# Kernel optimization log

Measured on AMD Instinct MI355X. Metric: run time of the kernel, lower is better.

The kernel has to match this reference:

```python
import jax, jax.numpy as jnp
import numpy as np

EPSILON = 0.01            # params.epsilon (cluster precision regularizer)
GAMMA = 0.005             # params.gamma (outlier/uniform component weight)
FIX_CLUSTER_POS_ITER = 1  # params.fix_cluster_pos_iter


def _sqdist(TVs, X):
    # TVs: (M, 3, N) transformed points, X: (K, 3) cluster means -> (M, N, K)
    return ((TVs ** 2).sum(1)[:, :, None]
            + (X ** 2).sum(1)[None, None, :]
            - 2.0 * jnp.einsum('mdn,kd->mnk', TVs, X))


def setup_inputs() -> dict:
    key = jax.random.key(0)
    kV, kX, kQ = jax.random.split(key, 3)
    M, N, K = 8, 8192, 256
    Vs = jax.random.normal(kV, (M, 3, N), dtype=jnp.float32)      # 3D point clouds
    X0 = jax.random.normal(kX, (K, 3), dtype=jnp.float32)         # init cluster means (sphere init)
    Q0 = 0.1 + 0.2 * jax.random.uniform(kQ, (K,), dtype=jnp.float32)  # init cluster precisions
    return {"Vs": Vs, "X0": X0, "Q0": Q0, "num_iters": 6}


def reference(Vs, X0, Q0, num_iters):
    M, _, N = Vs.shape
    K = X0.shape[0]
    dtype = Vs.dtype

    # mean_init: init_R = I, init_t = -mean(V) per view
    t0 = -Vs.mean(axis=2, keepdims=True)          # (M, 3, 1)
    TVs = Vs + t0
    beta = GAMMA * jnp.mean(Q0) ** 1.5            # get_default_beta(Q, gamma)

    X, Q = X0, Q0
    ds = _sqdist(TVs, X)                          # (M, N, K)
    R = jnp.broadcast_to(jnp.eye(3, dtype=dtype), (M, 3, 3))
    t = t0[:, :, 0]

    for i in range(num_iters):
        if i != num_iters - 1:  # detach everything except backprop_iter = [last]
            X = jax.lax.stop_gradient(X)
            Q = jax.lax.stop_gradient(Q)
            ds = jax.lax.stop_gradient(ds)

        # E-step: soft posteriors with uniform outlier component beta
        ap = jnp.exp(-0.5 * ds * Q) * Q ** 1.5    # (M, N, K); priors = 1, pyz_feature = 1
        a = ap / (ap.sum(axis=-1, keepdims=True) + beta)

        # M-step: weighted sufficient statistics
        L = a.sum(axis=1)                                   # (M, K)
        W = jnp.einsum('mdn,mnk->mdk', Vs, a) * Q           # (M, 3, K)
        mW = W.sum(axis=-1)                                 # (M, 3)
        b = L * Q                                           # (M, K)
        mX = jnp.einsum('mk,kd->md', b, X)                  # (M, 3)
        z = b.sum(axis=-1)                                  # (M,)

        # P = (W @ X)^T - mX mW^T / z  : 3x3 weighted cross-covariance per view
        P = (jnp.einsum('mdk,ke->med', W, X)
             - mX[:, :, None] * mW[:, None, :] / z[:, None, None])

        # batched Procrustes: R = U diag(1,1,det(U V^T)) V^T
        U, _, Vt = jnp.linalg.svd(P)
        det = jnp.linalg.det(jnp.einsum('mij,mjk->mik', U, Vt))
        sgn = jnp.concatenate([jnp.ones((M, 2), dtype), det[:, None]], axis=1)
        R = jnp.einsum('mij,mjk->mik', U * sgn[:, None, :], Vt)   # (M, 3, 3)
        t = (mX - jnp.einsum('mij,mj->mi', R, mW)) / z[:, None]   # (M, 3)
        TVs = jnp.einsum('mij,mjn->min', R, Vs) + t[:, :, None]   # (M, 3, N)

        # shared cluster updates (sum over views)
        den = L.sum(axis=0)                                 # (K,)
        if i > FIX_CLUSTER_POS_ITER:
            X = jnp.einsum('mdn,mnk->kd', TVs, a) / den[:, None]
        ds = _sqdist(TVs, X)
        wn = (a * ds).sum(axis=(0, 1))                      # (K,)
        Q = 3.0 * den / (wn + 3.0 * den * EPSILON)

    return TVs, R, t, X
```

## Files before the change

kernel.cpp:

```cpp
#include <hip/hip_runtime.h>
#include <math.h>

#define Mv 8
#define Nv 8192
#define Kv 256
#define BPM 64
#define NBLK (Mv*BPM)
#define NITER 6
#define EPSILON_C 0.01f
#define GAMMA_C 0.005f

#define WS_R     0
#define WS_T     72
#define WS_X     96
#define WS_Q     864
#define WS_BETA  1120
#define WS_ACC   1124
#define AC_STATS 0
#define AC_L     128
#define AC_W     2176
#define AC_H     8320
#define ACCSZ    10368

__device__ __forceinline__ float wave_red_sum(float x) {
  int v;
  float t;
  v = __builtin_bit_cast(int, x);
  t = __builtin_bit_cast(float, __builtin_amdgcn_update_dpp(0, v, 0x111, 0xf, 0xf, true));
  x += t; v = __builtin_bit_cast(int, x);
  t = __builtin_bit_cast(float, __builtin_amdgcn_update_dpp(0, v, 0x112, 0xf, 0xf, true));
  x += t; v = __builtin_bit_cast(int, x);
  t = __builtin_bit_cast(float, __builtin_amdgcn_update_dpp(0, v, 0x114, 0xf, 0xf, true));
  x += t; v = __builtin_bit_cast(int, x);
  t = __builtin_bit_cast(float, __builtin_amdgcn_update_dpp(0, v, 0x118, 0xf, 0xf, true));
  x += t; v = __builtin_bit_cast(int, x);
  t = __builtin_bit_cast(float, __builtin_amdgcn_update_dpp(0, v, 0x142, 0xa, 0xf, false));
  x += t; v = __builtin_bit_cast(int, x);
  t = __builtin_bit_cast(float, __builtin_amdgcn_update_dpp(0, v, 0x143, 0xc, 0xf, false));
  x += t;
  return __builtin_bit_cast(float, __builtin_amdgcn_readlane(__builtin_bit_cast(int, x), 63));
}

__global__ __launch_bounds__(256) void p0_init(const float* __restrict__ Vs,
                                               const float* __restrict__ X0,
                                               const float* __restrict__ Q0,
                                               float* __restrict__ ws) {
  __shared__ float sred[4];
  int tid = threadIdx.x;
  int b = blockIdx.x;
  int wave = tid >> 6, lane = tid & 63;
  if (b < 24) {
    int m = b / 3, d = b % 3;
    const float* src = Vs + (size_t)(m*3 + d) * Nv;
    float s = 0.f;
    for (int n = tid; n < Nv; n += 256) s += src[n];
    s = wave_red_sum(s);
    if (lane == 0) sred[wave] = s;
    __syncthreads();
    if (tid == 0) {
      float tot = sred[0]+sred[1]+sred[2]+sred[3];
      ws[WS_T + m*3 + d] = -tot / (float)Nv;
    }
    if (d == 0 && tid < 9) {
      ws[WS_R + m*9 + tid] = (tid==0||tid==4||tid==8) ? 1.f : 0.f;
    }
  } else {
    float s = (tid < Kv) ? Q0[tid] : 0.f;
    s = wave_red_sum(s);
    if (lane == 0) sred[wave] = s;
    __syncthreads();
    if (tid == 0) {
      float mq = (sred[0]+sred[1]+sred[2]+sred[3]) / (float)Kv;
      ws[WS_BETA] = GAMMA_C * mq * sqrtf(mq);
    }
    if (tid < Kv) ws[WS_Q + tid] = Q0[tid];
    for (int i = tid; i < Kv*3; i += 256) ws[WS_X + i] = X0[i];
    for (int i = tid; i < ACCSZ; i += 256) ws[WS_ACC + i] = 0.f;
  }
}

#define JROTF(app,aqq,apq,apr,aqr, vp0,vp1,vp2, vq0,vq1,vq2) do {           \
    float tau_ = (aqq - app) * __builtin_amdgcn_rcpf(2.0f*apq);             \
    float tt_ = __builtin_amdgcn_rcpf(fabsf(tau_) +                         \
                   __builtin_amdgcn_sqrtf(fmaf(tau_,tau_,1.0f)));           \
    tt_ = (tau_ < 0.0f) ? -tt_ : tt_;                                       \
    tt_ = (apq == 0.0f) ? 0.0f : tt_;                                       \
    float c_ = __builtin_amdgcn_rsqf(fmaf(tt_,tt_,1.0f)), s_ = tt_*c_;      \
    float papq_ = apq;                                                      \
    app = fmaf(-tt_,papq_,app); aqq = fmaf(tt_,papq_,aqq); apq = 0.0f;      \
    float tp_ = apr, tq_ = aqr;                                             \
    apr = c_*tp_ - s_*tq_; aqr = s_*tp_ + c_*tq_;                           \
    tp_=vp0; tq_=vq0; vp0=c_*tp_-s_*tq_; vq0=s_*tp_+c_*tq_;                 \
    tp_=vp1; tq_=vq1; vp1=c_*tp_-s_*tq_; vq1=s_*tp_+c_*tq_;                 \
    tp_=vp2; tq_=vq2; vp2=c_*tp_-s_*tq_; vq2=s_*tp_+c_*tq_;                 \
  } while(0)

#define CSWAP3F(la,lb, a0,a1,a2, b0,b1,b2) do {                             \
    if (la < lb) { float t_;                                                \
      t_=la; la=lb; lb=t_; t_=a0; a0=b0; b0=t_;                             \
      t_=a1; a1=b1; b1=t_; t_=a2; a2=b2; b2=t_; }                           \
  } while(0)

template<int ITPREV>
__device__ __forceinline__ void small_update(const float* __restrict__ acc,
                                             const float* __restrict__ ws,
                                             int tid,
                                             float (*sX)[3], float* sQ,
                                             float (*sR)[9], float (*sT)[3],
                                             float* sTn) {
  const int k = tid;
  float lk[Mv], w0v[Mv], w1v[Mv], w2v[Mv], hk[Mv];
  #pragma unroll
  for (int mm=0;mm<Mv;mm++) {
    lk[mm]  = acc[AC_L + mm*Kv + k];
    w0v[mm] = acc[AC_W + (mm*3+0)*Kv + k];
    w1v[mm] = acc[AC_W + (mm*3+1)*Kv + k];
    w2v[mm] = acc[AC_W + (mm*3+2)*Kv + k];
    hk[mm]  = acc[AC_H + mm*Kv + k];
  }
  float xp0 = 0.f, xp1 = 0.f, xp2 = 0.f;
  if (ITPREV <= 1) {
    xp0 = ws[WS_X + k*3+0]; xp1 = ws[WS_X + k*3+1]; xp2 = ws[WS_X + k*3+2];
  }

  if (tid < Mv) {
    int mm = tid;
    const float* st = acc + AC_STATS + mm*16;
    float s0=st[0], s1=st[1], s2v=st[2], s3=st[3], s4=st[4], s5=st[5],
          s6=st[6], s7=st[7], s8=st[8], s9=st[9], s10=st[10], s11=st[11],
          s12=st[12], s13=st[13], s14=st[14], s15=st[15];
    float z = s0;
    float mX0 = s1, mX1 = s2v, mX2 = s3;
    float mW0 = s4, mW1 = s5, mW2 = s6;
    float iz = __builtin_amdgcn_rcpf(z);
    float P00 = s7  - mX0*mW0*iz;
    float P01 = s8  - mX0*mW1*iz;
    float P02 = s9  - mX0*mW2*iz;
    float P10 = s10 - mX1*mW0*iz;
    float P11 = s11 - mX1*mW1*iz;
    float P12 = s12 - mX1*mW2*iz;
    float P20 = s13 - mX2*mW0*iz;
    float P21 = s14 - mX2*mW1*iz;
    float P22 = s15 - mX2*mW2*iz;
    float a00 = P00*P00 + P10*P10 + P20*P20;
    float a01 = P00*P01 + P10*P11 + P20*P21;
    float a02 = P00*P02 + P10*P12 + P20*P22;
    float a11 = P01*P01 + P11*P11 + P21*P21;
    float a12 = P01*P02 + P11*P12 + P21*P22;
    float a22 = P02*P02 + P12*P12 + P22*P22;
    float v00=1, v01=0, v02=0, v10=0, v11=1, v12=0, v20=0, v21=0, v22=1;
    #pragma unroll 1
    for (int sweep = 0; sweep < 8; sweep++) {
      JROTF(a00,a11,a01, a02,a12, v00,v10,v20, v01,v11,v21);
      JROTF(a00,a22,a02, a01,a12, v00,v10,v20, v02,v12,v22);
      JROTF(a11,a22,a12, a01,a02, v01,v11,v21, v02,v12,v22);
    }
    float l0 = a00, l1 = a11, l2 = a22;
    CSWAP3F(l0,l1, v00,v10,v20, v01,v11,v21);
    CSWAP3F(l1,l2, v01,v11,v21, v02,v12,v22);
    CSWAP3F(l0,l1, v00,v10,v20, v01,v11,v21);
    float detP = P00*(P11*P22-P12*P21) - P01*(P10*P22-P12*P20)
               + P02*(P10*P21-P11*P20);
    float s2d = (detP < 0.0f) ? -1.0f : 1.0f;
    float tiny = 1e-18f*l0 + 1e-30f;
    float w0i = __builtin_amdgcn_rsqf(fmaxf(l0,tiny));
    float w1i = __builtin_amdgcn_rsqf(fmaxf(l1,tiny));
    float w2i = s2d*__builtin_amdgcn_rsqf(fmaxf(l2,tiny));
    float M00 = w0i*v00*v00 + w1i*v01*v01 + w2i*v02*v02;
    float M01 = w0i*v00*v10 + w1i*v01*v11 + w2i*v02*v12;
    float M02 = w0i*v00*v20 + w1i*v01*v21 + w2i*v02*v22;
    float M11 = w0i*v10*v10 + w1i*v11*v11 + w2i*v12*v12;
    float M12 = w0i*v10*v20 + w1i*v11*v21 + w2i*v12*v22;
    float M22 = w0i*v20*v20 + w1i*v21*v21 + w2i*v22*v22;
    float R00n = P00*M00 + P01*M01 + P02*M02;
    float R01n = P00*M01 + P01*M11 + P02*M12;
    float R02n = P00*M02 + P01*M12 + P02*M22;
    float R10n = P10*M00 + P11*M01 + P12*M02;
    float R11n = P10*M01 + P11*M11 + P12*M12;
    float R12n = P10*M02 + P11*M12 + P12*M22;
    float R20n = P20*M00 + P21*M01 + P22*M02;
    float R21n = P20*M01 + P21*M11 + P22*M12;
    float R22n = P20*M02 + P21*M12 + P22*M22;
    float tm0 = (mX0 - (R00n*mW0 + R01n*mW1 + R02n*mW2))*iz;
    float tm1 = (mX1 - (R10n*mW0 + R11n*mW1 + R12n*mW2))*iz;
    float tm2 = (mX2 - (R20n*mW0 + R21n*mW1 + R22n*mW2))*iz;
    sR[mm][0]=R00n; sR[mm][1]=R01n; sR[mm][2]=R02n;
    sR[mm][3]=R10n; sR[mm][4]=R11n; sR[mm][5]=R12n;
    sR[mm][6]=R20n; sR[mm][7]=R21n; sR[mm][8]=R22n;
    sT[mm][0]=tm0; sT[mm][1]=tm1; sT[mm][2]=tm2;
    sTn[mm] = tm0*tm0 + tm1*tm1 + tm2*tm2;
  }
  __syncthreads();
  {
    float den = 0.f, Xn0=0.f, Xn1=0.f, Xn2=0.f, S2=0.f;
    #pragma unroll
    for (int mm=0;mm<Mv;mm++) {
      float r0 = sR[mm][0]*w0v[mm] + sR[mm][1]*w1v[mm] + sR[mm][2]*w2v[mm];
      float r1 = sR[mm][3]*w0v[mm] + sR[mm][4]*w1v[mm] + sR[mm][5]*w2v[mm];
      float r2 = sR[mm][6]*w0v[mm] + sR[mm][7]*w1v[mm] + sR[mm][8]*w2v[mm];
      float tt0 = sT[mm][0], tt1 = sT[mm][1], tt2 = sT[mm][2];
      den += lk[mm];
      Xn0 += r0 + tt0*lk[mm]; Xn1 += r1 + tt1*lk[mm]; Xn2 += r2 + tt2*lk[mm];
      S2  += hk[mm] + 2.f*(tt0*r0+tt1*r1+tt2*r2) + sTn[mm]*lk[mm];
    }
    float x0, x1, x2;
    if (ITPREV > 1) { float inv = __builtin_amdgcn_rcpf(den);
                      x0=Xn0*inv; x1=Xn1*inv; x2=Xn2*inv; }
    else            { x0=xp0; x1=xp1; x2=xp2; }
    float wn = S2 + (x0*x0+x1*x1+x2*x2)*den - 2.f*(x0*Xn0+x1*Xn1+x2*Xn2);
    float qn = 3.f*den / (wn + 3.f*den*EPSILON_C);
    sX[k][0]=x0; sX[k][1]=x1; sX[k][2]=x2;
    sQ[k] = qn;
  }
}

template<int IT>
__global__ __launch_bounds__(256) void p_iter(const float* __restrict__ Vs,
                                              float* __restrict__ ws) {
  __shared__ float sb[4][5][Kv];
  __shared__ float st4[4][16];
  __shared__ float sX[Kv][3];
  __shared__ float sQ[Kv];
  __shared__ float sR[Mv][9];
  __shared__ float sT[Mv][3];
  __shared__ float sTn[Mv];

  int tid  = threadIdx.x;
  int wave = tid >> 6, lane = tid & 63;
  int bid  = blockIdx.x;
  int m    = bid / BPM;
  int blk  = bid % BPM;
  int wid  = blk*4 + wave;
  const int k = tid;

  float* acc  = ws + WS_ACC + (IT % 3)*ACCSZ;
  float* accz = ws + WS_ACC + ((IT+1) % 3)*ACCSZ;
  float beta = ws[WS_BETA];

  if (IT == 0) {
    if (tid < 72) ((float*)sR)[tid] = ws[WS_R + tid];
    if (tid < 24) ((float*)sT)[tid] = ws[WS_T + tid];
    sX[k][0] = ws[WS_X + 3*k+0];
    sX[k][1] = ws[WS_X + 3*k+1];
    sX[k][2] = ws[WS_X + 3*k+2];
    sQ[k]    = ws[WS_Q + k];
  } else {
    const float* accp = ws + WS_ACC + ((IT+2) % 3)*ACCSZ;
    small_update<(IT > 0) ? (IT-1) : 0>(accp, ws, tid, sX, sQ, sR, sT, sTn);
  }
  __syncthreads();

  { int base = bid*21;
    if (tid < 21 && base + tid < ACCSZ) accz[base + tid] = 0.f; }

  float R00=sR[m][0],R01=sR[m][1],R02=sR[m][2];
  float R10=sR[m][3],R11=sR[m][4],R12=sR[m][5];
  float R20=sR[m][6],R21=sR[m][7],R22=sR[m][8];
  float t0=sT[m][0], t1=sT[m][1], t2=sT[m][2];
  float kXx[4],kXy[4],kXz[4],kA[4],kB[4],kQ[4],kQ32[4];
  #pragma unroll
  for (int j=0;j<4;j++) {
    int kk = lane + 64*j;
    float xx = sX[kk][0], xy = sX[kk][1], xz = sX[kk][2];
    float q  = sQ[kk];
    kXx[j]=xx; kXy[j]=xy; kXz[j]=xz;
    kA[j]  = -0.5f*q;
    kB[j]  = kA[j]*(xx*xx+xy*xy+xz*xz);
    kQ[j]  = q;
    kQ32[j]= q*sqrtf(q);
  }
  float aL[4]={0,0,0,0}, aWx[4]={0,0,0,0}, aWy[4]={0,0,0,0},
        aWz[4]={0,0,0,0}, aH[4]={0,0,0,0};
  const float* V0 = Vs + (size_t)(m*3+0)*Nv;
  const float* V1 = Vs + (size_t)(m*3+1)*Nv;
  const float* V2 = Vs + (size_t)(m*3+2)*Nv;
  for (int n = wid; n < Nv; n += 256) {
    float vx = V0[n], vy = V1[n], vz = V2[n];
    float px = fmaf(R00,vx, fmaf(R01,vy, fmaf(R02,vz, t0)));
    float py = fmaf(R10,vx, fmaf(R11,vy, fmaf(R12,vz, t1)));
    float pz = fmaf(R20,vx, fmaf(R21,vy, fmaf(R22,vz, t2)));
    float tvn = fmaf(px,px, fmaf(py,py, pz*pz));
    float vn  = fmaf(vx,vx, fmaf(vy,vy, vz*vz));
    float ap[4]; float s = 0.f;
    #pragma unroll
    for (int j=0;j<4;j++) {
      float dot = fmaf(px,kXx[j], fmaf(py,kXy[j], pz*kXz[j]));
      float arg = fmaf(kQ[j], dot, fmaf(kA[j], tvn, kB[j]));
      float e = __expf(arg)*kQ32[j];
      ap[j] = e; s += e;
    }
    float S = wave_red_sum(s);
    float inv = __builtin_amdgcn_rcpf(S + beta);
    #pragma unroll
    for (int j=0;j<4;j++) {
      float a = ap[j]*inv;
      aL[j] += a;
      aWx[j] = fmaf(a,vx,aWx[j]);
      aWy[j] = fmaf(a,vy,aWy[j]);
      aWz[j] = fmaf(a,vz,aWz[j]);
      aH[j]  = fmaf(a,vn,aH[j]);
    }
  }
  #pragma unroll
  for (int j=0;j<4;j++) {
    int kk = lane + 64*j;
    sb[wave][0][kk]=aL[j];  sb[wave][1][kk]=aWx[j]; sb[wave][2][kk]=aWy[j];
    sb[wave][3][kk]=aWz[j]; sb[wave][4][kk]=aH[j];
  }
  __syncthreads();
  const int k2 = (tid + 4*blk) & (Kv-1);
  float vL  = sb[0][0][k2]+sb[1][0][k2]+sb[2][0][k2]+sb[3][0][k2];
  float vWx = sb[0][1][k2]+sb[1][1][k2]+sb[2][1][k2]+sb[3][1][k2];
  float vWy = sb[0][2][k2]+sb[1][2][k2]+sb[2][2][k2]+sb[3][2][k2];
  float vWz = sb[0][3][k2]+sb[1][3][k2]+sb[2][3][k2]+sb[3][3][k2];
  float vH  = sb[0][4][k2]+sb[1][4][k2]+sb[2][4][k2]+sb[3][4][k2];
  atomicAdd(&acc[AC_L + m*Kv + k2], vL);
  atomicAdd(&acc[AC_W + (m*3+0)*Kv + k2], vWx);
  atomicAdd(&acc[AC_W + (m*3+1)*Kv + k2], vWy);
  atomicAdd(&acc[AC_W + (m*3+2)*Kv + k2], vWz);
  atomicAdd(&acc[AC_H + m*Kv + k2], vH);
  {
    float q  = sQ[k2];
    float x0 = sX[k2][0], x1 = sX[k2][1], x2 = sX[k2][2];
    float bk = vL*q;
    float sw0 = vWx*q, sw1 = vWy*q, sw2 = vWz*q;
    float pr[16];
    pr[0]=bk;  pr[1]=bk*x0; pr[2]=bk*x1; pr[3]=bk*x2;
    pr[4]=sw0; pr[5]=sw1;   pr[6]=sw2;
    pr[7]=sw0*x0;  pr[8]=sw1*x0;  pr[9]=sw2*x0;
    pr[10]=sw0*x1; pr[11]=sw1*x1; pr[12]=sw2*x1;
    pr[13]=sw0*x2; pr[14]=sw1*x2; pr[15]=sw2*x2;
    float red[16];
    #pragma unroll
    for (int v2=0; v2<16; v2++) red[v2] = wave_red_sum(pr[v2]);
    if (lane == 0) {
      #pragma unroll
      for (int v2=0; v2<16; v2++) st4[wave][v2] = red[v2];
    }
    __syncthreads();
    if (tid < 16)
      atomicAdd(&acc[AC_STATS + m*16 + ((tid + blk) & 15)],
                st4[0][(tid+blk)&15]+st4[1][(tid+blk)&15]+
                st4[2][(tid+blk)&15]+st4[3][(tid+blk)&15]);
  }
}

#define OUT_TOTAL (Mv*3*Nv + 72 + 24 + Kv*3)
__global__ __launch_bounds__(256) void p3_final(const float* __restrict__ Vs,
                                                const float* __restrict__ ws,
                                                float* __restrict__ out) {
  __shared__ float sX[Kv][3];
  __shared__ float sQ[Kv];
  __shared__ float sR[Mv][9];
  __shared__ float sT[Mv][3];
  __shared__ float sTn[Mv];
  int tid = threadIdx.x;
  const float* acc = ws + WS_ACC + ((NITER-1) % 3)*ACCSZ;
  small_update<NITER-1>(acc, ws, tid, sX, sQ, sR, sT, sTn);
  __syncthreads();

  for (int idx = blockIdx.x*256 + tid; idx < OUT_TOTAL; idx += 256*256) {
    if (idx < Mv*3*Nv) {
      int m = idx / (3*Nv);
      int r = idx % (3*Nv);
      int d = r / Nv;
      int n = r % Nv;
      float vx = Vs[(size_t)(m*3+0)*Nv + n];
      float vy = Vs[(size_t)(m*3+1)*Nv + n];
      float vz = Vs[(size_t)(m*3+2)*Nv + n];
      out[idx] = fmaf(sR[m][d*3+0],vx,
                 fmaf(sR[m][d*3+1],vy,
                 fmaf(sR[m][d*3+2],vz, sT[m][d])));
    } else {
      int j = idx - Mv*3*Nv;
      float v;
      if (j < 72)      v = ((float*)sR)[j];
      else if (j < 96) v = ((float*)sT)[j-72];
      else             v = ((float*)sX)[j-96];
      out[idx] = v;
    }
  }
}

extern "C" void kernel_launch(void* const* d_in, const int* in_sizes, int n_in,
                              void* d_out, int out_size, void* d_ws, size_t ws_size,
                              hipStream_t stream) {
  const float* Vs = (const float*)d_in[0];
  const float* X0 = (const float*)d_in[1];
  const float* Q0 = (const float*)d_in[2];
  float* out = (float*)d_out;
  float* ws  = (float*)d_ws;

  p0_init<<<25, 256, 0, stream>>>(Vs, X0, Q0, ws);
  p_iter<0><<<NBLK, 256, 0, stream>>>(Vs, ws);
  p_iter<1><<<NBLK, 256, 0, stream>>>(Vs, ws);
  p_iter<2><<<NBLK, 256, 0, stream>>>(Vs, ws);
  p_iter<3><<<NBLK, 256, 0, stream>>>(Vs, ws);
  p_iter<4><<<NBLK, 256, 0, stream>>>(Vs, ws);
  p_iter<5><<<NBLK, 256, 0, stream>>>(Vs, ws);
  p3_final<<<256, 256, 0, stream>>>(Vs, ws, out);
}
```

Baseline: 214.0 us.

## Double blocks per view, process two points per iteration, fold log2e into constants

Raises blocks per view from 64 to 128 and adds an occupancy hint to the launch bounds. The point loop now handles two points per iteration so their wave reductions and exp calls can interleave. The exp is rewritten as a native exp2 with log2(e) and Q folded into the per-cluster constants, which drops a multiply per cluster. More blocks means more atomic traffic into the accumulators and a smaller per-block zeroing slice; the two-point loop assumes N divides evenly by the stride.

```diff
diff --git a/kernel.cpp b/kernel.cpp
--- a/kernel.cpp
+++ b/kernel.cpp
@@ -4,8 +4,9 @@
 #define Mv 8
 #define Nv 8192
 #define Kv 256
-#define BPM 64
+#define BPM 128
 #define NBLK (Mv*BPM)
+#define WSTRIDE (4*BPM)
 #define NITER 6
 #define EPSILON_C 0.01f
 #define GAMMA_C 0.005f
@@ -215,8 +216,8 @@
 }
 
 template<int IT>
-__global__ __launch_bounds__(256) void p_iter(const float* __restrict__ Vs,
-                                              float* __restrict__ ws) {
+__global__ __launch_bounds__(256, 4) void p_iter(const float* __restrict__ Vs,
+                                                 float* __restrict__ ws) {
   __shared__ float sb[4][5][Kv];
   __shared__ float st4[4][16];
   __shared__ float sX[Kv][3];
@@ -230,7 +231,7 @@
   int bid  = blockIdx.x;
   int m    = bid / BPM;
   int blk  = bid % BPM;
-  int wid  = blk*4 + wave;
+  int wid  = __builtin_amdgcn_readfirstlane(blk*4 + wave);
   const int k = tid;
 
   float* acc  = ws + WS_ACC + (IT % 3)*ACCSZ;
@@ -250,23 +251,24 @@
   }
   __syncthreads();
 
-  { int base = bid*21;
-    if (tid < 21 && base + tid < ACCSZ) accz[base + tid] = 0.f; }
+  { int base = bid*11;
+    if (tid < 11 && base + tid < ACCSZ) accz[base + tid] = 0.f; }
 
   float R00=sR[m][0],R01=sR[m][1],R02=sR[m][2];
   float R10=sR[m][3],R11=sR[m][4],R12=sR[m][5];
   float R20=sR[m][6],R21=sR[m][7],R22=sR[m][8];
   float t0=sT[m][0], t1=sT[m][1], t2=sT[m][2];
-  float kXx[4],kXy[4],kXz[4],kA[4],kB[4],kQ[4],kQ32[4];
+  const float L2E = 1.4426950408889634f;
+  float kXx[4],kXy[4],kXz[4],kA[4],kB[4],kQ32[4];
   #pragma unroll
   for (int j=0;j<4;j++) {
     int kk = lane + 64*j;
     float xx = sX[kk][0], xy = sX[kk][1], xz = sX[kk][2];
     float q  = sQ[kk];
-    kXx[j]=xx; kXy[j]=xy; kXz[j]=xz;
-    kA[j]  = -0.5f*q;
+    float qL = q * L2E;
+    kA[j]  = -0.5f*qL;
+    kXx[j] = qL*xx; kXy[j] = qL*xy; kXz[j] = qL*xz;
     kB[j]  = kA[j]*(xx*xx+xy*xy+xz*xz);
-    kQ[j]  = q;
     kQ32[j]= q*sqrtf(q);
   }
   float aL[4]={0,0,0,0}, aWx[4]={0,0,0,0}, aWy[4]={0,0,0,0},
@@ -274,31 +276,48 @@
   const float* V0 = Vs + (size_t)(m*3+0)*Nv;
   const float* V1 = Vs + (size_t)(m*3+1)*Nv;
   const float* V2 = Vs + (size_t)(m*3+2)*Nv;
-  for (int n = wid; n < Nv; n += 256) {
-    float vx = V0[n], vy = V1[n], vz = V2[n];
-    float px = fmaf(R00,vx, fmaf(R01,vy, fmaf(R02,vz, t0)));
-    float py = fmaf(R10,vx, fmaf(R11,vy, fmaf(R12,vz, t1)));
-    float pz = fmaf(R20,vx, fmaf(R21,vy, fmaf(R22,vz, t2)));
-    float tvn = fmaf(px,px, fmaf(py,py, pz*pz));
-    float vn  = fmaf(vx,vx, fmaf(vy,vy, vz*vz));
-    float ap[4]; float s = 0.f;
+  #pragma unroll 1
+  for (int i = 0; i < Nv/(2*WSTRIDE); i++) {
+    int n0 = wid + (2*WSTRIDE)*i;
+    int n1 = n0 + WSTRIDE;
+    float vx0 = V0[n0], vy0 = V1[n0], vz0 = V2[n0];
+    float vx1 = V0[n1], vy1 = V1[n1], vz1 = V2[n1];
+    float px0 = fmaf(R00,vx0, fmaf(R01,vy0, fmaf(R02,vz0, t0)));
+    float py0 = fmaf(R10,vx0, fmaf(R11,vy0, fmaf(R12,vz0, t1)));
+    float pz0 = fmaf(R20,vx0, fmaf(R21,vy0, fmaf(R22,vz0, t2)));
+    float px1 = fmaf(R00,vx1, fmaf(R01,vy1, fmaf(R02,vz1, t0)));
+    float py1 = fmaf(R10,vx1, fmaf(R11,vy1, fmaf(R12,vz1, t1)));
+    float pz1 = fmaf(R20,vx1, fmaf(R21,vy1, fmaf(R22,vz1, t2)));
+    float tvn0 = fmaf(px0,px0, fmaf(py0,py0, pz0*pz0));
+    float tvn1 = fmaf(px1,px1, fmaf(py1,py1, pz1*pz1));
+    float vn0  = fmaf(vx0,vx0, fmaf(vy0,vy0, vz0*vz0));
+    float vn1  = fmaf(vx1,vx1, fmaf(vy1,vy1, vz1*vz1));
+    float ap0[4], ap1[4];
+    float s0 = 0.f, s1 = 0.f;
     #pragma unroll
     for (int j=0;j<4;j++) {
-      float dot = fmaf(px,kXx[j], fmaf(py,kXy[j], pz*kXz[j]));
-      float arg = fmaf(kQ[j], dot, fmaf(kA[j], tvn, kB[j]));
-      float e = __expf(arg)*kQ32[j];
-      ap[j] = e; s += e;
-    }
-    float S = wave_red_sum(s);
-    float inv = __builtin_amdgcn_rcpf(S + beta);
+      float b0 = fmaf(kA[j], tvn0, kB[j]);
+      float b1 = fmaf(kA[j], tvn1, kB[j]);
+      float arg0 = fmaf(px0,kXx[j], fmaf(py0,kXy[j], fmaf(pz0,kXz[j], b0)));
+      float arg1 = fmaf(px1,kXx[j], fmaf(py1,kXy[j], fmaf(pz1,kXz[j], b1)));
+      float e0 = __builtin_amdgcn_exp2f(arg0) * kQ32[j];
+      float e1 = __builtin_amdgcn_exp2f(arg1) * kQ32[j];
+      ap0[j] = e0; s0 += e0;
+      ap1[j] = e1; s1 += e1;
+    }
+    float S0 = wave_red_sum(s0);
+    float S1 = wave_red_sum(s1);
+    float inv0 = __builtin_amdgcn_rcpf(S0 + beta);
+    float inv1 = __builtin_amdgcn_rcpf(S1 + beta);
     #pragma unroll
     for (int j=0;j<4;j++) {
-      float a = ap[j]*inv;
-      aL[j] += a;
-      aWx[j] = fmaf(a,vx,aWx[j]);
-      aWy[j] = fmaf(a,vy,aWy[j]);
-      aWz[j] = fmaf(a,vz,aWz[j]);
-      aH[j]  = fmaf(a,vn,aH[j]);
+      float a0 = ap0[j]*inv0;
+      float a1 = ap1[j]*inv1;
+      aL[j] += a0 + a1;
+      aWx[j] = fmaf(a1,vx1, fmaf(a0,vx0, aWx[j]));
+      aWy[j] = fmaf(a1,vy1, fmaf(a0,vy0, aWy[j]));
+      aWz[j] = fmaf(a1,vz1, fmaf(a0,vz0, aWz[j]));
+      aH[j]  = fmaf(a1,vn1, fmaf(a0,vn0, aH[j]));
     }
   }
   #pragma unroll
```

After: 226.3 us. 1.06x slower.

## Restructure E-step to per-point normalizer pass then per-cluster accumulation

Applied to the files above, without the earlier changes.

Replaces the wave-per-point layout, where each lane held four clusters and a cross-lane reduction ran per point, with two phases per block. In the first phase each thread owns one point and loops over all clusters read from shared memory to compute its normalizer. In the second phase each thread owns one cluster and loops over the block's points to accumulate its statistics. This removes the per-point wave reductions and the shared-memory cross-wave combine, and switches to exp2 with folded constants. In exchange the exponential is computed twice per point-cluster pair, and the block count is halved to 32 blocks per view with 256 points each.

```diff
diff --git a/kernel.cpp b/kernel.cpp
--- a/kernel.cpp
+++ b/kernel.cpp
@@ -4,8 +4,9 @@
 #define Mv 8
 #define Nv 8192
 #define Kv 256
-#define BPM 64
+#define BPM 32
 #define NBLK (Mv*BPM)
+#define NPB (Nv/BPM)
 #define NITER 6
 #define EPSILON_C 0.01f
 #define GAMMA_C 0.005f
@@ -217,7 +218,10 @@
 template<int IT>
 __global__ __launch_bounds__(256) void p_iter(const float* __restrict__ Vs,
                                               float* __restrict__ ws) {
-  __shared__ float sb[4][5][Kv];
+  __shared__ __align__(16) float sC[Kv][8];
+  __shared__ __align__(16) float sPT[NPB][4];
+  __shared__ __align__(16) float sVV[NPB][4];
+  __shared__ float sInv[NPB];
   __shared__ float st4[4][16];
   __shared__ float sX[Kv][3];
   __shared__ float sQ[Kv];
@@ -230,8 +234,7 @@
   int bid  = blockIdx.x;
   int m    = bid / BPM;
   int blk  = bid % BPM;
-  int wid  = blk*4 + wave;
-  const int k = tid;
+  int n0   = blk * NPB;
 
   float* acc  = ws + WS_ACC + (IT % 3)*ACCSZ;
   float* accz = ws + WS_ACC + ((IT+1) % 3)*ACCSZ;
@@ -240,96 +243,101 @@
   if (IT == 0) {
     if (tid < 72) ((float*)sR)[tid] = ws[WS_R + tid];
     if (tid < 24) ((float*)sT)[tid] = ws[WS_T + tid];
-    sX[k][0] = ws[WS_X + 3*k+0];
-    sX[k][1] = ws[WS_X + 3*k+1];
-    sX[k][2] = ws[WS_X + 3*k+2];
-    sQ[k]    = ws[WS_Q + k];
+    sX[tid][0] = ws[WS_X + 3*tid+0];
+    sX[tid][1] = ws[WS_X + 3*tid+1];
+    sX[tid][2] = ws[WS_X + 3*tid+2];
+    sQ[tid]    = ws[WS_Q + tid];
   } else {
     const float* accp = ws + WS_ACC + ((IT+2) % 3)*ACCSZ;
     small_update<(IT > 0) ? (IT-1) : 0>(accp, ws, tid, sX, sQ, sR, sT, sTn);
   }
   __syncthreads();
 
-  { int base = bid*21;
-    if (tid < 21 && base + tid < ACCSZ) accz[base + tid] = 0.f; }
+  { int base = bid*41;
+    if (tid < 41 && base + tid < ACCSZ) accz[base + tid] = 0.f; }
+
+  const float L2E = 1.4426950408889634f;
+  float xx = sX[tid][0], xy = sX[tid][1], xz = sX[tid][2];
+  float q  = sQ[tid];
+  float qL   = q * L2E;
+  float kA   = -0.5f*qL;
+  float kXx  = qL*xx, kXy = qL*xy, kXz = qL*xz;
+  float kB   = kA*(xx*xx+xy*xy+xz*xz);
+  float kQ32 = q*sqrtf(q);
+  sC[tid][0]=kXx; sC[tid][1]=kXy; sC[tid][2]=kXz;
+  sC[tid][3]=kA;  sC[tid][4]=kB;  sC[tid][5]=kQ32;
 
   float R00=sR[m][0],R01=sR[m][1],R02=sR[m][2];
   float R10=sR[m][3],R11=sR[m][4],R12=sR[m][5];
   float R20=sR[m][6],R21=sR[m][7],R22=sR[m][8];
   float t0=sT[m][0], t1=sT[m][1], t2=sT[m][2];
-  float kXx[4],kXy[4],kXz[4],kA[4],kB[4],kQ[4],kQ32[4];
-  #pragma unroll
-  for (int j=0;j<4;j++) {
-    int kk = lane + 64*j;
-    float xx = sX[kk][0], xy = sX[kk][1], xz = sX[kk][2];
-    float q  = sQ[kk];
-    kXx[j]=xx; kXy[j]=xy; kXz[j]=xz;
-    kA[j]  = -0.5f*q;
-    kB[j]  = kA[j]*(xx*xx+xy*xy+xz*xz);
-    kQ[j]  = q;
-    kQ32[j]= q*sqrtf(q);
-  }
-  float aL[4]={0,0,0,0}, aWx[4]={0,0,0,0}, aWy[4]={0,0,0,0},
-        aWz[4]={0,0,0,0}, aH[4]={0,0,0,0};
-  const float* V0 = Vs + (size_t)(m*3+0)*Nv;
-  const float* V1 = Vs + (size_t)(m*3+1)*Nv;
-  const float* V2 = Vs + (size_t)(m*3+2)*Nv;
-  for (int n = wid; n < Nv; n += 256) {
-    float vx = V0[n], vy = V1[n], vz = V2[n];
-    float px = fmaf(R00,vx, fmaf(R01,vy, fmaf(R02,vz, t0)));
-    float py = fmaf(R10,vx, fmaf(R11,vy, fmaf(R12,vz, t1)));
-    float pz = fmaf(R20,vx, fmaf(R21,vy, fmaf(R22,vz, t2)));
-    float tvn = fmaf(px,px, fmaf(py,py, pz*pz));
-    float vn  = fmaf(vx,vx, fmaf(vy,vy, vz*vz));
-    float ap[4]; float s = 0.f;
-    #pragma unroll
-    for (int j=0;j<4;j++) {
-      float dot = fmaf(px,kXx[j], fmaf(py,kXy[j], pz*kXz[j]));
-      float arg = fmaf(kQ[j], dot, fmaf(kA[j], tvn, kB[j]));
-      float e = __expf(arg)*kQ32[j];
-      ap[j] = e; s += e;
-    }
-    float S = wave_red_sum(s);
-    float inv = __builtin_amdgcn_rcpf(S + beta);
-    #pragma unroll
-    for (int j=0;j<4;j++) {
-      float a = ap[j]*inv;
-      aL[j] += a;
-      aWx[j] = fmaf(a,vx,aWx[j]);
-      aWy[j] = fmaf(a,vy,aWy[j]);
-      aWz[j] = fmaf(a,vz,aWz[j]);
-      aH[j]  = fmaf(a,vn,aH[j]);
-    }
-  }
-  #pragma unroll
-  for (int j=0;j<4;j++) {
-    int kk = lane + 64*j;
-    sb[wave][0][kk]=aL[j];  sb[wave][1][kk]=aWx[j]; sb[wave][2][kk]=aWy[j];
-    sb[wave][3][kk]=aWz[j]; sb[wave][4][kk]=aH[j];
-  }
+  int n = n0 + tid;
+  float vx = Vs[(size_t)(m*3+0)*Nv + n];
+  float vy = Vs[(size_t)(m*3+1)*Nv + n];
+  float vz = Vs[(size_t)(m*3+2)*Nv + n];
+  float px = fmaf(R00,vx, fmaf(R01,vy, fmaf(R02,vz, t0)));
+  float py = fmaf(R10,vx, fmaf(R11,vy, fmaf(R12,vz, t1)));
+  float pz = fmaf(R20,vx, fmaf(R21,vy, fmaf(R22,vz, t2)));
+  float tvn = fmaf(px,px, fmaf(py,py, pz*pz));
+  float vn  = fmaf(vx,vx, fmaf(vy,vy, vz*vz));
+  sPT[tid][0]=px; sPT[tid][1]=py; sPT[tid][2]=pz; sPT[tid][3]=tvn;
+  sVV[tid][0]=vx; sVV[tid][1]=vy; sVV[tid][2]=vz; sVV[tid][3]=vn;
   __syncthreads();
-  const int k2 = (tid + 4*blk) & (Kv-1);
-  float vL  = sb[0][0][k2]+sb[1][0][k2]+sb[2][0][k2]+sb[3][0][k2];
-  float vWx = sb[0][1][k2]+sb[1][1][k2]+sb[2][1][k2]+sb[3][1][k2];
-  float vWy = sb[0][2][k2]+sb[1][2][k2]+sb[2][2][k2]+sb[3][2][k2];
-  float vWz = sb[0][3][k2]+sb[1][3][k2]+sb[2][3][k2]+sb[3][3][k2];
-  float vH  = sb[0][4][k2]+sb[1][4][k2]+sb[2][4][k2]+sb[3][4][k2];
-  atomicAdd(&acc[AC_L + m*Kv + k2], vL);
-  atomicAdd(&acc[AC_W + (m*3+0)*Kv + k2], vWx);
-  atomicAdd(&acc[AC_W + (m*3+1)*Kv + k2], vWy);
-  atomicAdd(&acc[AC_W + (m*3+2)*Kv + k2], vWz);
-  atomicAdd(&acc[AC_H + m*Kv + k2], vH);
+
   {
-    float q  = sQ[k2];
-    float x0 = sX[k2][0], x1 = sX[k2][1], x2 = sX[k2][2];
-    float bk = vL*q;
-    float sw0 = vWx*q, sw1 = vWy*q, sw2 = vWz*q;
+    float s0=0.f, s1=0.f, s2=0.f, s3=0.f;
+    #pragma unroll 2
+    for (int k = 0; k < Kv; k += 4) {
+      float4 c0 = *reinterpret_cast<const float4*>(&sC[k+0][0]);
+      float2 d0 = *reinterpret_cast<const float2*>(&sC[k+0][4]);
+      float4 c1 = *reinterpret_cast<const float4*>(&sC[k+1][0]);
+      float2 d1 = *reinterpret_cast<const float2*>(&sC[k+1][4]);
+      float4 c2 = *reinterpret_cast<const float4*>(&sC[k+2][0]);
+      float2 d2 = *reinterpret_cast<const float2*>(&sC[k+2][4]);
+      float4 c3 = *reinterpret_cast<const float4*>(&sC[k+3][0]);
+      float2 d3 = *reinterpret_cast<const float2*>(&sC[k+3][4]);
+      float a0 = fmaf(px,c0.x, fmaf(py,c0.y, fmaf(pz,c0.z, fmaf(c0.w,tvn,d0.x))));
+      float a1 = fmaf(px,c1.x, fmaf(py,c1.y, fmaf(pz,c1.z, fmaf(c1.w,tvn,d1.x))));
+      float a2 = fmaf(px,c2.x, fmaf(py,c2.y, fmaf(pz,c2.z, fmaf(c2.w,tvn,d2.x))));
+      float a3 = fmaf(px,c3.x, fmaf(py,c3.y, fmaf(pz,c3.z, fmaf(c3.w,tvn,d3.x))));
+      s0 = fmaf(__builtin_amdgcn_exp2f(a0), d0.y, s0);
+      s1 = fmaf(__builtin_amdgcn_exp2f(a1), d1.y, s1);
+      s2 = fmaf(__builtin_amdgcn_exp2f(a2), d2.y, s2);
+      s3 = fmaf(__builtin_amdgcn_exp2f(a3), d3.y, s3);
+    }
+    sInv[tid] = __builtin_amdgcn_rcpf(((s0+s1)+(s2+s3)) + beta);
+  }
+  __syncthreads();
+
+  float aL=0.f, aWx=0.f, aWy=0.f, aWz=0.f, aH=0.f;
+  #pragma unroll 4
+  for (int nn = 0; nn < NPB; nn++) {
+    float4 p = *reinterpret_cast<const float4*>(&sPT[nn][0]);
+    float4 v = *reinterpret_cast<const float4*>(&sVV[nn][0]);
+    float iv = sInv[nn];
+    float arg = fmaf(kXx,p.x, fmaf(kXy,p.y, fmaf(kXz,p.z, fmaf(kA,p.w,kB))));
+    float a = __builtin_amdgcn_exp2f(arg) * (kQ32*iv);
+    aL += a;
+    aWx = fmaf(a,v.x,aWx);
+    aWy = fmaf(a,v.y,aWy);
+    aWz = fmaf(a,v.z,aWz);
+    aH  = fmaf(a,v.w,aH);
+  }
+  atomicAdd(&acc[AC_L + m*Kv + tid], aL);
+  atomicAdd(&acc[AC_W + (m*3+0)*Kv + tid], aWx);
+  atomicAdd(&acc[AC_W + (m*3+1)*Kv + tid], aWy);
+  atomicAdd(&acc[AC_W + (m*3+2)*Kv + tid], aWz);
+  atomicAdd(&acc[AC_H + m*Kv + tid], aH);
+
+  {
+    float bk = aL*q;
+    float sw0 = aWx*q, sw1 = aWy*q, sw2 = aWz*q;
     float pr[16];
-    pr[0]=bk;  pr[1]=bk*x0; pr[2]=bk*x1; pr[3]=bk*x2;
+    pr[0]=bk;  pr[1]=bk*xx; pr[2]=bk*xy; pr[3]=bk*xz;
     pr[4]=sw0; pr[5]=sw1;   pr[6]=sw2;
-    pr[7]=sw0*x0;  pr[8]=sw1*x0;  pr[9]=sw2*x0;
-    pr[10]=sw0*x1; pr[11]=sw1*x1; pr[12]=sw2*x1;
-    pr[13]=sw0*x2; pr[14]=sw1*x2; pr[15]=sw2*x2;
+    pr[7]=sw0*xx;  pr[8]=sw1*xx;  pr[9]=sw2*xx;
+    pr[10]=sw0*xy; pr[11]=sw1*xy; pr[12]=sw2*xy;
+    pr[13]=sw0*xz; pr[14]=sw1*xz; pr[15]=sw2*xz;
     float red[16];
     #pragma unroll
     for (int v2=0; v2<16; v2++) red[v2] = wave_red_sum(pr[v2]);
```

Result: faster. 207.7 us (-2.9%).
